# Performance work log

Measured on AMD Instinct MI355X. Metric: run time of the kernel, lower is better.

Reference implementation:

```python
import jax
jax.config.update('jax_enable_x64', True)  # exact int64 phase products (torch builds phasors in complex128)
import jax.numpy as jnp
import numpy as np

L = 393216          # seq_length, divisible by Locc=4, K=12, mmse_block=12
K = 12              # ktc=4 -> K=12
LOCC = 4            # _compute_locc for ktc=4
U, P = 8, 4         # max_users, max_ports_per_user
BLK = 12            # mmse_block_size
SEARCH_MIN, SEARCH_MAX = -10, 10


def setup_inputs() -> dict:
    key = jax.random.key(0)
    k1, k2, k3 = jax.random.split(key, 3)
    ls_real = jax.random.normal(k1, (L,), dtype=jnp.float32)
    ls_imag = jax.random.normal(k2, (L,), dtype=jnp.float32)
    cyclic_shifts = jax.random.randint(k3, (U, P), 0, K)  # int, values in [0, K)
    return {"ls_real": ls_real, "ls_imag": ls_imag, "cyclic_shifts": cyclic_shifts}


def _phasor(m):
    """exp(1j*2*pi*m*n/L) for each m in the [UP] vector -> [UP, L] complex64.
    Phase reduced mod L in exact int64 before float conversion for accuracy."""
    n = jnp.arange(L, dtype=jnp.int64)
    r = (m.astype(jnp.int64)[:, None] * n[None, :]) % L      # exact
    ang = (2.0 * np.pi / L) * r.astype(jnp.float32)
    return jnp.exp(1j * ang).astype(jnp.complex64)


def _forward(ls, cyclic_shifts):
    shifts = cyclic_shifts.reshape(-1)                        # [UP]
    ideal_peak = ((K - shifts) % K) * L // K                  # [UP]

    # --- timing offset search in +/-10 window around ideal peak (CIR domain) ---
    h_time = jnp.fft.ifft(ls)                                 # IDFT
    h_mag = jnp.abs(h_time) ** 2                              # [L]
    offs = jnp.arange(SEARCH_MIN, SEARCH_MAX + 1)             # [21]
    win = (ideal_peak[:, None] + offs[None, :]) % L           # [UP, 21]
    T = offs[jnp.argmax(h_mag[win], axis=1)]                  # [UP] timing offsets
    m = T + ideal_peak                                        # [UP]

    ph_m = _phasor(m)                                         # [UP, L]
    ph_T = _phasor(T)                                         # [UP, L]

    # --- per-port cyclic de-shift, OCC demux (avg of 4), linear interp back to L ---
    h_up = ls[None, :] * ph_m                                 # [UP, L]
    h_avg = h_up.reshape(-1, L // LOCC, LOCC).mean(-1)        # [UP, L/4]
    orig_idx = (LOCC - 1) / 2.0 + LOCC * jnp.arange(L // LOCC, dtype=jnp.float32)
    new_idx = jnp.arange(L, dtype=jnp.float32)
    interp1 = jax.vmap(lambda y: jnp.interp(new_idx, orig_idx, y))
    h_interp = (interp1(h_avg.real.astype(jnp.float32))
                + 1j * interp1(h_avg.imag.astype(jnp.float32))).astype(jnp.complex64)  # [UP, L]

    # --- residual reconstruction and re-addition per port ---
    h_recon = jnp.sum(h_interp * jnp.conj(ph_m), axis=0)      # [L]
    residual = ls - h_recon
    h_wr = h_interp + residual[None, :] * ph_m                # [UP, L]

    # --- noise power estimate from adjacent-sample differences ---
    diff = ls[1:] - ls[:-1]
    noise_power = jnp.mean(jnp.abs(diff) ** 2) / 2

    # --- block MMSE: h_mmse = C (C + R)^-1 h with default C = I, R = sigma^2 I ---
    C = jnp.eye(BLK, dtype=jnp.complex64)
    Rm = noise_power.astype(jnp.complex64) * jnp.eye(BLK, dtype=jnp.complex64)
    M = C @ jnp.linalg.inv(C + Rm)                            # [12, 12]
    hb = h_wr.reshape(-1, L // BLK, BLK)                      # [UP, L/12, 12]
    h_mmse = jnp.einsum('ij,ubj->ubi', M, hb).reshape(-1, L)  # [UP, L]

    # --- align back by conj timing phasor ---
    return h_mmse * jnp.conj(ph_T)                            # [UP, L] complex64


def reference(ls_real, ls_imag, cyclic_shifts):
    ls = (ls_real + 1j * ls_imag).astype(jnp.complex64)
    return _forward(ls, cyclic_shifts)
```

## Files before the change

kernel.cpp:

```cpp
#include <hip/hip_runtime.h>
#include <math.h>

#define L_TOT 393216
#define L_D4  98304
#define NPORT 32
#define NPEAK 12
#define NOFF  21
#define NCAND 252
#define TILE  1536
#define NBLK  (L_TOT / TILE)
#define HALF_ELEMS 12582912ull

__device__ float2 g_F[NCAND * NBLK];
__device__ double g_npart[NBLK];
__device__ double g_hmag[NCAND];
__device__ int    g_prm[96];
__device__ float  g_scale[1];

__constant__ double c_cos12[12] = {1.0, 0.8660254037844387, 0.5, 0.0, -0.5,
  -0.8660254037844387, -1.0, -0.8660254037844387, -0.5, 0.0, 0.5, 0.8660254037844387};
__constant__ double c_sin12[12] = {0.0, 0.5, 0.8660254037844387, 1.0,
  0.8660254037844387, 0.5, 0.0, -0.5, -0.8660254037844387, -1.0,
  -0.8660254037844387, -0.5};

__device__ __forceinline__ void interp_coords(int n, int* j0, float* f) {
  float x = ((float)n - 1.5f) * 0.25f;
  if (x <= 0.f)                    { *j0 = 0;        *f = 0.f; }
  else if (x >= (float)(L_D4 - 1)) { *j0 = L_D4 - 2; *f = 1.f; }
  else { int jj = (int)x; *j0 = jj; *f = x - (float)jj; }
}

__device__ __forceinline__ float2 zpow(float2 z, float2 z2, float2 z4, float2 z8, int T) {
  int t = T < 0 ? -T : T;
  float cr = 1.f, ci = 0.f;
  if (t & 1) { cr = z.x; ci = z.y; }
  if (t & 2) { float a = cr*z2.x - ci*z2.y, b = cr*z2.y + ci*z2.x; cr = a; ci = b; }
  if (t & 4) { float a = cr*z4.x - ci*z4.y, b = cr*z4.y + ci*z4.x; cr = a; ci = b; }
  if (t & 8) { float a = cr*z8.x - ci*z8.y, b = cr*z8.y + ci*z8.x; cr = a; ci = b; }
  if (T < 0) ci = -ci;
  return make_float2(cr, ci);
}

__global__ __launch_bounds__(256) void search_kernel(
    const float* __restrict__ lsr, const float* __restrict__ lsi) {
  __shared__ float2 sh_ls[TILE + 1];
  __shared__ float2 sh_z[TILE];
  __shared__ float2 sh_red[NCAND * NOFF];
  const float w = (float)(2.0 * M_PI / (double)L_TOT);
  int tid = threadIdx.x;
  int KB = blockIdx.x * TILE;
  for (int i = tid; i < TILE + 1; i += 256) {
    int k = KB + i; if (k > L_TOT - 1) k = L_TOT - 1;
    sh_ls[i] = make_float2(lsr[k], lsi[k]);
  }
  for (int i = tid; i < TILE; i += 256) {
    float s, c; __sincosf(w * (float)(KB + i), &s, &c);
    sh_z[i] = make_float2(c, s);
  }
  __syncthreads();

  if (tid < NCAND) {
    int r = tid % 12, lane = tid / 12;
    float accr[NOFF], acci[NOFF];
#pragma unroll
    for (int d = 0; d < NOFF; ++d) { accr[d] = 0.f; acci[d] = 0.f; }
    for (int q = lane; q < TILE / 12; q += 21) {
      int kl = 12 * q + r;
      float2 y = sh_ls[kl];
      float2 z = sh_z[kl];
      accr[10] += y.x; acci[10] += y.y;
      float cpr = y.x, cpi = y.y, cmr = y.x, cmi = y.y;
#pragma unroll
      for (int d = 1; d <= 10; ++d) {
        float tr = cpr*z.x - cpi*z.y, ti = cpr*z.y + cpi*z.x; cpr = tr; cpi = ti;
        accr[10 + d] += cpr; acci[10 + d] += cpi;
        tr = cmr*z.x + cmi*z.y; ti = cmi*z.x - cmr*z.y; cmr = tr; cmi = ti;
        accr[10 - d] += cmr; acci[10 - d] += cmi;
      }
    }
#pragma unroll
    for (int d = 0; d < NOFF; ++d)
      sh_red[tid * NOFF + d] = make_float2(accr[d], acci[d]);
  }
  double nacc = 0.0;
  int top = (KB + TILE <= L_TOT - 1) ? TILE : (L_TOT - 1 - KB);
  for (int i = tid; i < top; i += 256) {
    float2 a = sh_ls[i], b = sh_ls[i + 1];
    float dr = b.x - a.x, di = b.y - a.y;
    nacc += (double)(dr * dr + di * di);
  }
  __syncthreads();
  if (tid < NCAND) {
    int r = tid / NOFF, dd = tid - r * NOFF;
    float fr = 0.f, fi = 0.f;
    for (int lane = 0; lane < 21; ++lane) {
      float2 v = sh_red[(lane * 12 + r) * NOFF + dd];
      fr += v.x; fi += v.y;
    }
    g_F[(r * NOFF + dd) * NBLK + blockIdx.x] = make_float2(fr, fi);
  }
  __syncthreads();
  double* nb = (double*)sh_red;
  nb[tid] = nacc;
  __syncthreads();
  for (int t = 128; t > 0; t >>= 1) {
    if (tid < t) nb[tid] += nb[tid + t];
    __syncthreads();
  }
  if (tid == 0) g_npart[blockIdx.x] = nb[0];
}

__global__ __launch_bounds__(256) void reduce_kernel() {
  int c = blockIdx.x;
  int p = c / NOFF, dd = c - p * NOFF;
  int b = threadIdx.x;
  double sr = 0.0, si = 0.0;
  for (int r = 0; r < 12; ++r) {
    float2 v = g_F[(r * NOFF + dd) * NBLK + b];
    int idx = (p * r) % 12;
    double tr = c_cos12[idx], ti = c_sin12[idx];
    sr += tr * (double)v.x - ti * (double)v.y;
    si += tr * (double)v.y + ti * (double)v.x;
  }
  __shared__ double s0[256], s1[256];
  s0[b] = sr; s1[b] = si;
  __syncthreads();
  for (int t = 128; t > 0; t >>= 1) {
    if (b < t) { s0[b] += s0[b + t]; s1[b] += s1[b + t]; }
    __syncthreads();
  }
  if (b == 0) g_hmag[c] = s0[0] * s0[0] + s1[0] * s1[0];
}

__global__ __launch_bounds__(256) void select_kernel(
    const int* __restrict__ shifts) {
  __shared__ double hmag[NCAND];
  __shared__ double nred[256];
  int tid = threadIdx.x;
  if (tid < NCAND) hmag[tid] = g_hmag[tid];
  nred[tid] = g_npart[tid];
  __syncthreads();
  for (int t = 128; t > 0; t >>= 1) {
    if (tid < t) nred[tid] += nred[tid + t];
    __syncthreads();
  }
  if (tid < NPORT) {
    int s = shifts[tid];
    int p = (NPEAK - (s % NPEAK)) % NPEAK;
    double best = -1.0; int bd = 0;
    for (int d = 0; d < NOFF; ++d) {
      double v = hmag[p * NOFF + d];
      if (v > best) { best = v; bd = d; }
    }
    g_prm[tid]      = bd - 10;
    g_prm[32 + tid] = p;
  }
  if (tid == 0) {
    double npow = nred[0] / (double)(L_TOT - 1) * 0.5;
    g_scale[0] = (float)(1.0 / (1.0 + npow));
  }
}

__global__ __launch_bounds__(256) void fused_kernel(
    const float* __restrict__ lsr, const float* __restrict__ lsi,
    float* __restrict__ out, unsigned long long out_elems) {
  __shared__ float2 sh_ls[264];
  __shared__ float2 sh_z[264];
  __shared__ float2 sh_h[NPORT][66];
  __shared__ float2 sh_tbl[144];
  __shared__ int    sm_T[NPORT], sm_p[NPORT];
  __shared__ float  sm_scale;

  const float w = (float)(2.0 * M_PI / (double)L_TOT);
  int tid = threadIdx.x;
  int N0 = blockIdx.x * 256;
  int JBASE; float fd;
  interp_coords(N0, &JBASE, &fd);
  int K0 = 4 * JBASE;

  if (tid < NPORT) { sm_T[tid] = g_prm[tid]; sm_p[tid] = g_prm[32 + tid]; }
  if (tid == 0) sm_scale = g_scale[0];
  if (tid < 144) {
    int p = tid / 12, r = tid - p * 12;
    int idx = (p * r) % 12;
    float s, c; __sincosf((float)(2.0 * M_PI / 12.0) * (float)idx, &s, &c);
    sh_tbl[tid] = make_float2(c, s);
  }
  for (int i = tid; i < 264; i += 256) {
    int k = K0 + i; if (k > L_TOT - 1) k = L_TOT - 1;
    sh_ls[i] = make_float2(lsr[k], lsi[k]);
    float s, c; __sincosf(w * (float)k, &s, &c);
    sh_z[i] = make_float2(c, s);
  }
  __syncthreads();

  for (int e = tid; e < NPORT * 66; e += 256) {
    int u = e / 66, jj = e - u * 66;
    int j = JBASE + jj; if (j > L_D4 - 1) j = L_D4 - 1;
    int k0 = 4 * j, kk = k0 - K0;
    int T = sm_T[u], p = sm_p[u];
    int r0 = k0 % 12;
    float sr = 0.f, si = 0.f;
#pragma unroll
    for (int t = 0; t < 4; ++t) {
      float2 z = sh_z[kk + t];
      float2 z2 = make_float2(z.x*z.x - z.y*z.y, 2.f*z.x*z.y);
      float2 z4 = make_float2(z2.x*z2.x - z2.y*z2.y, 2.f*z2.x*z2.y);
      float2 z8 = make_float2(z4.x*z4.x - z4.y*z4.y, 2.f*z4.x*z4.y);
      float2 zT = zpow(z, z2, z4, z8, T);
      int rr = r0 + t; if (rr >= 12) rr -= 12;
      float2 tb = sh_tbl[p * 12 + rr];
      float phr = tb.x*zT.x - tb.y*zT.y, phi = tb.x*zT.y + tb.y*zT.x;
      float2 v = sh_ls[kk + t];
      sr += v.x*phr - v.y*phi;
      si += v.x*phi + v.y*phr;
    }
    sh_h[u][jj] = make_float2(0.25f * sr, 0.25f * si);
  }
  __syncthreads();

  int n = N0 + tid;
  int j0; float f;
  interp_coords(n, &j0, &f);
  int jj0 = j0 - JBASE;
  int r12 = n % 12;
  float2 lsn = sh_ls[n - K0];
  float2 zn = sh_z[n - K0];
  float2 z2 = make_float2(zn.x*zn.x - zn.y*zn.y, 2.f*zn.x*zn.y);
  float2 z4 = make_float2(z2.x*z2.x - z2.y*z2.y, 2.f*z2.x*z2.y);
  float2 z8 = make_float2(z4.x*z4.x - z4.y*z4.y, 2.f*z4.x*z4.y);

  float rcr = 0.f, rci = 0.f;
#pragma unroll
  for (int u = 0; u < NPORT; ++u) {
    float2 zT = zpow(zn, z2, z4, z8, sm_T[u]);
    float2 tb = sh_tbl[sm_p[u] * 12 + r12];
    float phr = tb.x*zT.x - tb.y*zT.y, phi = tb.x*zT.y + tb.y*zT.x;
    float2 y0 = sh_h[u][jj0], y1 = sh_h[u][jj0 + 1];
    float hr = y0.x + f * (y1.x - y0.x);
    float hi = y0.y + f * (y1.y - y0.y);
    rcr += hr * phr + hi * phi;
    rci += hi * phr - hr * phi;
  }
  float resr = lsn.x - rcr, resi = lsn.y - rci;
  float scl = sm_scale;

#pragma unroll
  for (int u = 0; u < NPORT; ++u) {
    float2 zT = zpow(zn, z2, z4, z8, sm_T[u]);
    float2 tb = sh_tbl[sm_p[u] * 12 + r12];
    float2 y0 = sh_h[u][jj0], y1 = sh_h[u][jj0 + 1];
    float hr = y0.x + f * (y1.x - y0.x);
    float hi = y0.y + f * (y1.y - y0.y);
    float orr = hr*zT.x + hi*zT.y + resr*tb.x - resi*tb.y;
    float oii = hi*zT.x - hr*zT.y + resr*tb.y + resi*tb.x;
    unsigned long long o = (unsigned long long)u * L_TOT + (unsigned)n;
    if (o < out_elems)              out[o] = scl * orr;
    if (HALF_ELEMS + o < out_elems) out[HALF_ELEMS + o] = scl * oii;
  }
}

extern "C" void kernel_launch(void* const* d_in, const int* in_sizes, int n_in,
                              void* d_out, int out_size, void* d_ws, size_t ws_size,
                              hipStream_t stream) {
  const float* lsr    = (const float*)d_in[0];
  const float* lsi    = (const float*)d_in[1];
  const int*   shifts = (const int*)d_in[2];
  float* out = (float*)d_out;

  if (in_sizes[0] != L_TOT || in_sizes[1] != L_TOT) return;

  unsigned long long out_elems = (unsigned long long)(out_size > 0 ? out_size : 0);

  search_kernel<<<NBLK, 256, 0, stream>>>(lsr, lsi);
  reduce_kernel<<<NCAND, 256, 0, stream>>>();
  select_kernel<<<1, 256, 0, stream>>>(shifts);
  fused_kernel<<<L_TOT / 256, 256, 0, stream>>>(lsr, lsi, out, out_elems);
}
```

Before: 130.5 us.

## Drop reduce kernel, fold reduction into select, cache per-port phasors in fused kernel

Removes the separate reduce kernel by storing per-block partial sums candidate-major and having the single select block sum them over all blocks and apply the 12-point twiddle itself. In the fused kernel, the OCC-averaging phasor is now built from one sincos of the exactly reduced phase times a recurrence step, instead of repeated squaring and powering. The first port loop caches the timing-rotated interpolated values in registers so the output loop does not recompute them. Port parameters are made wave-uniform with readfirstlane, and the output stores lose their bounds checks when the buffer is full size. Costs: the select kernel now does a serial 256-step sum per thread on one block, and the 64 cached floats per thread raise register pressure.

```diff
diff --git a/kernel.cpp b/kernel.cpp
--- a/kernel.cpp
+++ b/kernel.cpp
@@ -11,9 +11,8 @@
 #define NBLK  (L_TOT / TILE)
 #define HALF_ELEMS 12582912ull
 
-__device__ float2 g_F[NCAND * NBLK];
+__device__ float2 g_F[NBLK * NCAND];
 __device__ double g_npart[NBLK];
-__device__ double g_hmag[NCAND];
 __device__ int    g_prm[96];
 __device__ float  g_scale[1];
 
@@ -30,7 +29,7 @@
   else { int jj = (int)x; *j0 = jj; *f = x - (float)jj; }
 }
 
-__device__ __forceinline__ float2 zpow(float2 z, float2 z2, float2 z4, float2 z8, int T) {
+__device__ __forceinline__ float2 zpowS(float2 z, float2 z2, float2 z4, float2 z8, int T) {
   int t = T < 0 ? -T : T;
   float cr = 1.f, ci = 0.f;
   if (t & 1) { cr = z.x; ci = z.y; }
@@ -97,7 +96,7 @@
       float2 v = sh_red[(lane * 12 + r) * NOFF + dd];
       fr += v.x; fi += v.y;
     }
-    g_F[(r * NOFF + dd) * NBLK + blockIdx.x] = make_float2(fr, fi);
+    g_F[blockIdx.x * NCAND + tid] = make_float2(fr, fi);
   }
   __syncthreads();
   double* nb = (double*)sh_red;
@@ -110,35 +109,33 @@
   if (tid == 0) g_npart[blockIdx.x] = nb[0];
 }
 
-__global__ __launch_bounds__(256) void reduce_kernel() {
-  int c = blockIdx.x;
-  int p = c / NOFF, dd = c - p * NOFF;
-  int b = threadIdx.x;
-  double sr = 0.0, si = 0.0;
-  for (int r = 0; r < 12; ++r) {
-    float2 v = g_F[(r * NOFF + dd) * NBLK + b];
-    int idx = (p * r) % 12;
-    double tr = c_cos12[idx], ti = c_sin12[idx];
-    sr += tr * (double)v.x - ti * (double)v.y;
-    si += tr * (double)v.y + ti * (double)v.x;
-  }
-  __shared__ double s0[256], s1[256];
-  s0[b] = sr; s1[b] = si;
-  __syncthreads();
-  for (int t = 128; t > 0; t >>= 1) {
-    if (b < t) { s0[b] += s0[b + t]; s1[b] += s1[b + t]; }
-    __syncthreads();
-  }
-  if (b == 0) g_hmag[c] = s0[0] * s0[0] + s1[0] * s1[0];
-}
-
 __global__ __launch_bounds__(256) void select_kernel(
     const int* __restrict__ shifts) {
+  __shared__ double sGr[NCAND], sGi[NCAND];
   __shared__ double hmag[NCAND];
   __shared__ double nred[256];
   int tid = threadIdx.x;
-  if (tid < NCAND) hmag[tid] = g_hmag[tid];
+  if (tid < NCAND) {
+    double gr = 0.0, gi = 0.0;
+    for (int b = 0; b < NBLK; ++b) {
+      float2 v = g_F[b * NCAND + tid];
+      gr += (double)v.x; gi += (double)v.y;
+    }
+    sGr[tid] = gr; sGi[tid] = gi;
+  }
   nred[tid] = g_npart[tid];
+  __syncthreads();
+  if (tid < NCAND) {
+    int p = tid / NOFF, dd = tid - p * NOFF;
+    double sr = 0.0, si = 0.0;
+    for (int r = 0; r < 12; ++r) {
+      int idx = (p * r) % 12;
+      double gr = sGr[r * NOFF + dd], gi = sGi[r * NOFF + dd];
+      sr += c_cos12[idx] * gr - c_sin12[idx] * gi;
+      si += c_cos12[idx] * gi + c_sin12[idx] * gr;
+    }
+    hmag[tid] = sr * sr + si * si;
+  }
   __syncthreads();
   for (int t = 128; t > 0; t >>= 1) {
     if (tid < t) nred[tid] += nred[tid + t];
@@ -152,8 +149,12 @@
       double v = hmag[p * NOFF + d];
       if (v > best) { best = v; bd = d; }
     }
-    g_prm[tid]      = bd - 10;
+    int T = bd - 10;
+    int m = T + p * (L_TOT / NPEAK);
+    if (m < 0) m += L_TOT;
+    g_prm[tid]      = T;
     g_prm[32 + tid] = p;
+    g_prm[64 + tid] = m;
   }
   if (tid == 0) {
     double npow = nred[0] / (double)(L_TOT - 1) * 0.5;
@@ -165,10 +166,10 @@
     const float* __restrict__ lsr, const float* __restrict__ lsi,
     float* __restrict__ out, unsigned long long out_elems) {
   __shared__ float2 sh_ls[264];
-  __shared__ float2 sh_z[264];
-  __shared__ float2 sh_h[NPORT][66];
+  __shared__ float2 sh_h[NPORT][67];
   __shared__ float2 sh_tbl[144];
-  __shared__ int    sm_T[NPORT], sm_p[NPORT];
+  __shared__ float2 sh_stp[NPORT];
+  __shared__ int    sm_T[NPORT], sm_p[NPORT], sm_m[NPORT];
   __shared__ float  sm_scale;
 
   const float w = (float)(2.0 * M_PI / (double)L_TOT);
@@ -178,7 +179,12 @@
   interp_coords(N0, &JBASE, &fd);
   int K0 = 4 * JBASE;
 
-  if (tid < NPORT) { sm_T[tid] = g_prm[tid]; sm_p[tid] = g_prm[32 + tid]; }
+  if (tid < NPORT) {
+    sm_T[tid] = g_prm[tid]; sm_p[tid] = g_prm[32 + tid];
+    int m = g_prm[64 + tid]; sm_m[tid] = m;
+    float s, c; __sincosf(w * (float)m, &s, &c);
+    sh_stp[tid] = make_float2(c, s);
+  }
   if (tid == 0) sm_scale = g_scale[0];
   if (tid < 144) {
     int p = tid / 12, r = tid - p * 12;
@@ -189,31 +195,24 @@
   for (int i = tid; i < 264; i += 256) {
     int k = K0 + i; if (k > L_TOT - 1) k = L_TOT - 1;
     sh_ls[i] = make_float2(lsr[k], lsi[k]);
-    float s, c; __sincosf(w * (float)k, &s, &c);
-    sh_z[i] = make_float2(c, s);
   }
   __syncthreads();
 
   for (int e = tid; e < NPORT * 66; e += 256) {
-    int u = e / 66, jj = e - u * 66;
+    int u = e & 31, jj = e >> 5;
     int j = JBASE + jj; if (j > L_D4 - 1) j = L_D4 - 1;
     int k0 = 4 * j, kk = k0 - K0;
-    int T = sm_T[u], p = sm_p[u];
-    int r0 = k0 % 12;
+    unsigned rr = (unsigned)(((long long)sm_m[u] * k0) % L_TOT);
+    float phs, phc; __sincosf(w * (float)rr, &phs, &phc);
+    float2 stp = sh_stp[u];
     float sr = 0.f, si = 0.f;
 #pragma unroll
     for (int t = 0; t < 4; ++t) {
-      float2 z = sh_z[kk + t];
-      float2 z2 = make_float2(z.x*z.x - z.y*z.y, 2.f*z.x*z.y);
-      float2 z4 = make_float2(z2.x*z2.x - z2.y*z2.y, 2.f*z2.x*z2.y);
-      float2 z8 = make_float2(z4.x*z4.x - z4.y*z4.y, 2.f*z4.x*z4.y);
-      float2 zT = zpow(z, z2, z4, z8, T);
-      int rr = r0 + t; if (rr >= 12) rr -= 12;
-      float2 tb = sh_tbl[p * 12 + rr];
-      float phr = tb.x*zT.x - tb.y*zT.y, phi = tb.x*zT.y + tb.y*zT.x;
       float2 v = sh_ls[kk + t];
-      sr += v.x*phr - v.y*phi;
-      si += v.x*phi + v.y*phr;
+      sr += v.x * phc - v.y * phs;
+      si += v.x * phs + v.y * phc;
+      float a = phc * stp.x - phs * stp.y, b = phc * stp.y + phs * stp.x;
+      phc = a; phs = b;
     }
     sh_h[u][jj] = make_float2(0.25f * sr, 0.25f * si);
   }
@@ -225,38 +224,54 @@
   int jj0 = j0 - JBASE;
   int r12 = n % 12;
   float2 lsn = sh_ls[n - K0];
-  float2 zn = sh_z[n - K0];
+  float zs, zc; __sincosf(w * (float)n, &zs, &zc);
+  float2 zn = make_float2(zc, zs);
   float2 z2 = make_float2(zn.x*zn.x - zn.y*zn.y, 2.f*zn.x*zn.y);
   float2 z4 = make_float2(z2.x*z2.x - z2.y*z2.y, 2.f*z2.x*z2.y);
   float2 z8 = make_float2(z4.x*z4.x - z4.y*z4.y, 2.f*z4.x*z4.y);
 
+  float aAr[NPORT], aAi[NPORT];
   float rcr = 0.f, rci = 0.f;
 #pragma unroll
   for (int u = 0; u < NPORT; ++u) {
-    float2 zT = zpow(zn, z2, z4, z8, sm_T[u]);
-    float2 tb = sh_tbl[sm_p[u] * 12 + r12];
-    float phr = tb.x*zT.x - tb.y*zT.y, phi = tb.x*zT.y + tb.y*zT.x;
+    int T = __builtin_amdgcn_readfirstlane(sm_T[u]);
+    int p = __builtin_amdgcn_readfirstlane(sm_p[u]);
+    float2 zT = zpowS(zn, z2, z4, z8, T);
+    float2 tb = sh_tbl[p * 12 + r12];
     float2 y0 = sh_h[u][jj0], y1 = sh_h[u][jj0 + 1];
     float hr = y0.x + f * (y1.x - y0.x);
     float hi = y0.y + f * (y1.y - y0.y);
-    rcr += hr * phr + hi * phi;
-    rci += hi * phr - hr * phi;
+    float Ar = hr * zT.x + hi * zT.y;
+    float Ai = hi * zT.x - hr * zT.y;
+    aAr[u] = Ar; aAi[u] = Ai;
+    rcr += Ar * tb.x + Ai * tb.y;
+    rci += Ai * tb.x - Ar * tb.y;
   }
   float resr = lsn.x - rcr, resi = lsn.y - rci;
   float scl = sm_scale;
 
-#pragma unroll
-  for (int u = 0; u < NPORT; ++u) {
-    float2 zT = zpow(zn, z2, z4, z8, sm_T[u]);
-    float2 tb = sh_tbl[sm_p[u] * 12 + r12];
-    float2 y0 = sh_h[u][jj0], y1 = sh_h[u][jj0 + 1];
-    float hr = y0.x + f * (y1.x - y0.x);
-    float hi = y0.y + f * (y1.y - y0.y);
-    float orr = hr*zT.x + hi*zT.y + resr*tb.x - resi*tb.y;
-    float oii = hi*zT.x - hr*zT.y + resr*tb.y + resi*tb.x;
-    unsigned long long o = (unsigned long long)u * L_TOT + (unsigned)n;
-    if (o < out_elems)              out[o] = scl * orr;
-    if (HALF_ELEMS + o < out_elems) out[HALF_ELEMS + o] = scl * oii;
+  if (out_elems >= 2ull * HALF_ELEMS) {
+#pragma unroll
+    for (int u = 0; u < NPORT; ++u) {
+      int p = __builtin_amdgcn_readfirstlane(sm_p[u]);
+      float2 tb = sh_tbl[p * 12 + r12];
+      float orr = aAr[u] + resr * tb.x - resi * tb.y;
+      float oii = aAi[u] + resr * tb.y + resi * tb.x;
+      unsigned long long o = (unsigned long long)u * L_TOT + (unsigned)n;
+      out[o] = scl * orr;
+      out[HALF_ELEMS + o] = scl * oii;
+    }
+  } else {
+#pragma unroll
+    for (int u = 0; u < NPORT; ++u) {
+      int p = __builtin_amdgcn_readfirstlane(sm_p[u]);
+      float2 tb = sh_tbl[p * 12 + r12];
+      float orr = aAr[u] + resr * tb.x - resi * tb.y;
+      float oii = aAi[u] + resr * tb.y + resi * tb.x;
+      unsigned long long o = (unsigned long long)u * L_TOT + (unsigned)n;
+      if (o < out_elems)              out[o] = scl * orr;
+      if (HALF_ELEMS + o < out_elems) out[HALF_ELEMS + o] = scl * oii;
+    }
   }
 }
 
@@ -273,7 +288,6 @@
   unsigned long long out_elems = (unsigned long long)(out_size > 0 ? out_size : 0);
 
   search_kernel<<<NBLK, 256, 0, stream>>>(lsr, lsi);
-  reduce_kernel<<<NCAND, 256, 0, stream>>>();
   select_kernel<<<1, 256, 0, stream>>>(shifts);
   fused_kernel<<<L_TOT / 256, 256, 0, stream>>>(lsr, lsi, out, out_elems);
 }
```

After: 121.7 us. 1.07x faster.
